# Kernel tuning notes

Hardware: AMD Instinct MI355X
Metric: run time of the kernel (lower is better)

## Reference

```python
import jax, jax.numpy as jnp
import numpy as np

N_STEPS = 8  # fixed-step Dormand-Prince RK45 steps replacing adaptive dopri5


def setup_inputs() -> dict:
    key = jax.random.key(0)
    ks = jax.random.split(key, 12)
    B, I, H = 16384, 128, 256
    s_ih = 1.0 / np.sqrt(I)
    s_hh = 1.0 / np.sqrt(H)
    return {
        "inputs": jax.random.normal(ks[0], (B, I), jnp.float32),
        "h0": jax.random.normal(ks[1], (B, H), jnp.float32),
        "c0": jax.random.normal(ks[2], (B, H), jnp.float32),
        "ts": jax.random.uniform(ks[3], (B,), jnp.float32),  # per-example end times in [0,1)
        "W_ih": jax.random.normal(ks[4], (4 * H, I), jnp.float32) * s_ih,
        "W_hh": jax.random.normal(ks[5], (4 * H, H), jnp.float32) * s_hh,
        "b_ih": jax.random.normal(ks[6], (4 * H,), jnp.float32) * s_hh,
        "b_hh": jax.random.normal(ks[7], (4 * H,), jnp.float32) * s_hh,
        "W1": jax.random.normal(ks[8], (H, H), jnp.float32) * s_hh,
        "b1": jax.random.normal(ks[9], (H,), jnp.float32) * s_hh,
        "W2": jax.random.normal(ks[10], (H, H), jnp.float32) * s_hh,
        "b2": jax.random.normal(ks[11], (H,), jnp.float32) * s_hh,
    }


def reference(inputs, h0, c0, ts, W_ih, W_hh, b_ih, b_hh, W1, b1, W2, b2):
    # ODE vector field: fc = Linear -> Tanh -> Linear (autonomous)
    def f(h):
        return jnp.tanh(h @ W1.T + b1) @ W2.T + b2

    dt = (ts / N_STEPS)[:, None]  # [B,1] per-example step size

    def rk45_step(h, _):
        k1 = f(h)
        k2 = f(h + dt * (0.2 * k1))
        k3 = f(h + dt * (3.0 / 40.0 * k1 + 9.0 / 40.0 * k2))
        k4 = f(h + dt * (44.0 / 45.0 * k1 - 56.0 / 15.0 * k2 + 32.0 / 9.0 * k3))
        k5 = f(h + dt * (19372.0 / 6561.0 * k1 - 25360.0 / 2187.0 * k2
                         + 64448.0 / 6561.0 * k3 - 212.0 / 729.0 * k4))
        k6 = f(h + dt * (9017.0 / 3168.0 * k1 - 355.0 / 33.0 * k2
                         + 46732.0 / 5247.0 * k3 + 49.0 / 176.0 * k4
                         - 5103.0 / 18656.0 * k5))
        h_new = h + dt * (35.0 / 384.0 * k1 + 500.0 / 1113.0 * k3
                          + 125.0 / 192.0 * k4 - 2187.0 / 6784.0 * k5
                          + 11.0 / 84.0 * k6)
        return h_new, None

    h_ode, _ = jax.lax.scan(rk45_step, h0, None, length=N_STEPS)

    def lstm_cell(x, h, c):
        gates = x @ W_ih.T + b_ih + h @ W_hh.T + b_hh  # [B,4H]
        i, fg, g, o = jnp.split(gates, 4, axis=-1)
        i = jax.nn.sigmoid(i)
        fg = jax.nn.sigmoid(fg)
        g = jnp.tanh(g)
        o = jax.nn.sigmoid(o)
        c_new = fg * c + i * g
        return o * jnp.tanh(c_new), c_new

    # two (weight-shared) LSTMCell applications as in the original forward
    h1, c1 = lstm_cell(inputs, h_ode, c0)
    h2, c2 = lstm_cell(inputs, h1, c1)
    return h2, c2
```

## Files before the change

kernel.cpp:

```cpp
#include <hip/hip_runtime.h>

#define B_TOT 16384
#define HD 256
#define ID 128
#define BT 32
#define NSTEP 8
#define YP 264
#define XP 136

typedef float    f32x4  __attribute__((ext_vector_type(4)));
typedef float    f32x16 __attribute__((ext_vector_type(16)));
typedef _Float16 f16x8  __attribute__((ext_vector_type(8)));
typedef _Float16 f16x4  __attribute__((ext_vector_type(4)));
typedef _Float16 f16x2  __attribute__((ext_vector_type(2)));

__device__ __forceinline__ float fast_rcp(float x){ return __builtin_amdgcn_rcpf(x); }
__device__ __forceinline__ float fast_exp2(float x){ return __builtin_amdgcn_exp2f(x); }
__device__ __forceinline__ float fast_tanh(float x){
  return 1.0f - 2.0f*fast_rcp(1.0f + fast_exp2(x*2.8853900817779268f));
}
__device__ __forceinline__ float fast_sigmoid(float x){
  return fast_rcp(1.0f + fast_exp2(x*-1.4426950408889634f));
}

__global__ void cvt_f32_f16(const float* __restrict__ src, _Float16* __restrict__ dst, int n4){
  int i = blockIdx.x*256 + threadIdx.x;
  if (i < n4){
    float4 v = ((const float4*)src)[i];
    f16x4 t = {(_Float16)v.x, (_Float16)v.y, (_Float16)v.z, (_Float16)v.w};
    *(f16x4*)(dst + (size_t)i*4) = t;
  }
}

#define KP(i) ((float)kpk[i][pk][hw])

__global__ __launch_bounds__(512, 2)
void ode_lstm(const float* __restrict__ inputs, const float* __restrict__ h0,
              const float* __restrict__ c0,     const float* __restrict__ ts,
              const float* __restrict__ b_ih,   const float* __restrict__ b_hh,
              const float* __restrict__ b1,     const float* __restrict__ b2,
              const _Float16* __restrict__ W1h, const _Float16* __restrict__ W2h,
              const _Float16* __restrict__ Wihh,const _Float16* __restrict__ Whhh,
              float* __restrict__ out)
{
  __shared__ __align__(16) _Float16 yl[BT*YP];
  __shared__ __align__(16) _Float16 ul[BT*YP];
  __shared__ __align__(16) _Float16 xl[BT*XP];
  __shared__ __align__(16) float b1l[HD], b2l[HD], bsl[4*HD];
  __shared__ float dtl[BT];

  const int tid  = threadIdx.x;
  const int wv   = tid >> 6;
  const int lane = tid & 63;
  const int l31  = lane & 31;
  const int hh   = lane >> 5;
  const int row0 = blockIdx.x * BT;
  const int cb   = wv*32 + hh*4;
  const int yrow = l31*YP + cb;

  #pragma unroll
  for (int it = 0; it < 2; ++it){
    int idx = tid + it*512;
    int r = idx >> 5, c4 = idx & 31;
    float4 v = ((const float4*)inputs)[(size_t)(row0 + r)*(ID/4) + c4];
    f16x4 t = {(_Float16)v.x, (_Float16)v.y, (_Float16)v.z, (_Float16)v.w};
    *(f16x4*)(xl + r*XP + c4*4) = t;
  }
  if (tid < HD){ b1l[tid] = b1[tid]; b2l[tid] = b2[tid]; }
  bsl[tid]       = b_ih[tid]       + b_hh[tid];
  bsl[tid + 512] = b_ih[tid + 512] + b_hh[tid + 512];
  if (tid < BT) dtl[tid] = ts[row0 + tid] * (1.0f/NSTEP);

  f16x8 W1f[16], W2f[16];
  {
    const _Float16* w1p = W1h + (size_t)(wv*32 + l31)*HD + hh*8;
    const _Float16* w2p = W2h + (size_t)(wv*32 + l31)*HD + hh*8;
    #pragma unroll
    for (int kt = 0; kt < 16; ++kt){
      W1f[kt] = *(const f16x8*)(w1p + kt*16);
      W2f[kt] = *(const f16x8*)(w2p + kt*16);
    }
  }

  f32x4 h4[4];
  #pragma unroll
  for (int g2 = 0; g2 < 4; ++g2){
    f32x4 hv = *(const f32x4*)(h0 + (size_t)(row0 + l31)*HD + cb + 8*g2);
    h4[g2] = hv;
    f16x4 t = {(_Float16)hv[0], (_Float16)hv[1], (_Float16)hv[2], (_Float16)hv[3]};
    *(f16x4*)(yl + yrow + 8*g2) = t;
  }
  __syncthreads();
  const float dtv = dtl[l31];

  auto gemm16 = [&](const f16x8 (&Wf)[16], const _Float16* __restrict__ act)->f32x16{
    f32x16 a = {};
    const _Float16* bp = act + l31*YP + hh*8;
    #pragma unroll
    for (int kt = 0; kt < 16; ++kt){
      f16x8 Bf = *(const f16x8*)(bp + kt*16);
      a = __builtin_amdgcn_mfma_f32_32x32x16_f16(Wf[kt], Bf, a, 0, 0, 0);
    }
    return a;
  };

  auto phase1 = [&](){
    f32x16 a = gemm16(W1f, yl);
    #pragma unroll
    for (int g2 = 0; g2 < 4; ++g2){
      f32x4 bv = *(const f32x4*)(b1l + cb + 8*g2);
      f16x4 uv;
      #pragma unroll
      for (int r3 = 0; r3 < 4; ++r3)
        uv[r3] = (_Float16)fast_tanh(a[g2*4 + r3] + bv[r3]);
      *(f16x4*)(ul + yrow + 8*g2) = uv;
    }
    __syncthreads();
  };

  #define STAGE(SIDX, YEXPR)                                              \
    phase1();                                                             \
    { f32x16 a2 = gemm16(W2f, ul);                                        \
      _Pragma("unroll")                                                   \
      for (int g2 = 0; g2 < 4; ++g2){                                     \
        f32x4 bv = *(const f32x4*)(b2l + cb + 8*g2);                      \
        f16x4 yv;                                                         \
        _Pragma("unroll")                                                 \
        for (int r3 = 0; r3 < 4; ++r3){                                   \
          const int r = g2*4 + r3; const int pk = r>>1; const int hw = r&1;\
          float kd = dtv*(a2[r] + bv[r3]);                                \
          if (SIDX < 5) kpk[SIDX][pk][hw] = (_Float16)kd;                 \
          yv[r3] = (_Float16)(YEXPR);                                     \
        }                                                                 \
        *(f16x4*)(yl + yrow + 8*g2) = yv;                                 \
      }                                                                   \
    }                                                                     \
    __syncthreads();

  #pragma unroll 1
  for (int step = 0; step < NSTEP; ++step){
    f16x2 kpk[5][8];

    STAGE(0, h4[g2][r3] + 0.2f*kd)
    STAGE(1, h4[g2][r3] + 0.075f*KP(0) + 0.225f*kd)
    STAGE(2, h4[g2][r3] + (44.0f/45.0f)*KP(0) + (-56.0f/15.0f)*KP(1)
                        + (32.0f/9.0f)*kd)
    STAGE(3, h4[g2][r3] + (19372.0f/6561.0f)*KP(0) + (-25360.0f/2187.0f)*KP(1)
                        + (64448.0f/6561.0f)*KP(2) + (-212.0f/729.0f)*kd)
    STAGE(4, h4[g2][r3] + (9017.0f/3168.0f)*KP(0) + (-355.0f/33.0f)*KP(1)
                        + (46732.0f/5247.0f)*KP(2) + (49.0f/176.0f)*KP(3)
                        + (-5103.0f/18656.0f)*kd)
    phase1();
    { f32x16 a2 = gemm16(W2f, ul);
      #pragma unroll
      for (int g2 = 0; g2 < 4; ++g2){
        f32x4 bv = *(const f32x4*)(b2l + cb + 8*g2);
        f16x4 yv;
        #pragma unroll
        for (int r3 = 0; r3 < 4; ++r3){
          const int r = g2*4 + r3; const int pk = r>>1; const int hw = r&1;
          float kd = dtv*(a2[r] + bv[r3]);
          float hn = h4[g2][r3] + (35.0f/384.0f)*KP(0) + (500.0f/1113.0f)*KP(2)
                   + (125.0f/192.0f)*KP(3) + (-2187.0f/6784.0f)*KP(4)
                   + (11.0f/84.0f)*kd;
          h4[g2][r3] = hn;
          yv[r3] = (_Float16)hn;
        }
        *(f16x4*)(yl + yrow + 8*g2) = yv;
      }
    }
    __syncthreads();
  }

  f32x16 agx[4] = {};
  {
    const _Float16* bp = xl + l31*XP + hh*8;
    #pragma unroll 2
    for (int kt = 0; kt < 8; ++kt){
      f16x8 Bf = *(const f16x8*)(bp + kt*16);
      #pragma unroll
      for (int g = 0; g < 4; ++g){
        f16x8 Af = *(const f16x8*)(Wihh + (size_t)(g*HD + wv*32 + l31)*ID + kt*16 + hh*8);
        agx[g] = __builtin_amdgcn_mfma_f32_32x32x16_f16(Af, Bf, agx[g], 0, 0, 0);
      }
    }
  }
  f32x4 c4[4];
  #pragma unroll
  for (int g2 = 0; g2 < 4; ++g2)
    c4[g2] = *(const f32x4*)(c0 + (size_t)(row0 + l31)*HD + cb + 8*g2);

  #pragma unroll 1
  for (int cell = 0; cell < 2; ++cell){
    f32x16 ag[4];
    #pragma unroll
    for (int g = 0; g < 4; ++g) ag[g] = agx[g];
    const _Float16* hsrc = (cell == 0) ? yl : ul;
    const _Float16* bp = hsrc + l31*YP + hh*8;
    #pragma unroll 2
    for (int kt = 0; kt < 16; ++kt){
      f16x8 Bf = *(const f16x8*)(bp + kt*16);
      #pragma unroll
      for (int g = 0; g < 4; ++g){
        f16x8 Af = *(const f16x8*)(Whhh + (size_t)(g*HD + wv*32 + l31)*HD + kt*16 + hh*8);
        ag[g] = __builtin_amdgcn_mfma_f32_32x32x16_f16(Af, Bf, ag[g], 0, 0, 0);
      }
    }
    #pragma unroll
    for (int g2 = 0; g2 < 4; ++g2){
      f32x4 bi = *(const f32x4*)(bsl + 0*HD + cb + 8*g2);
      f32x4 bf = *(const f32x4*)(bsl + 1*HD + cb + 8*g2);
      f32x4 bg = *(const f32x4*)(bsl + 2*HD + cb + 8*g2);
      f32x4 bo = *(const f32x4*)(bsl + 3*HD + cb + 8*g2);
      f16x4 hv; f32x4 ho, co;
      #pragma unroll
      for (int r3 = 0; r3 < 4; ++r3){
        const int r = g2*4 + r3;
        float iv = fast_sigmoid(ag[0][r] + bi[r3]);
        float fv = fast_sigmoid(ag[1][r] + bf[r3]);
        float gv = fast_tanh   (ag[2][r] + bg[r3]);
        float ov = fast_sigmoid(ag[3][r] + bo[r3]);
        float cn = fv*c4[g2][r3] + iv*gv;
        c4[g2][r3] = cn;
        float hn = ov*fast_tanh(cn);
        hv[r3] = (_Float16)hn; ho[r3] = hn; co[r3] = cn;
      }
      if (cell == 0){
        *(f16x4*)(ul + yrow + 8*g2) = hv;
      } else {
        size_t o = (size_t)(row0 + l31)*HD + cb + 8*g2;
        *(f32x4*)(out + o) = ho;
        *(f32x4*)(out + (size_t)B_TOT*HD + o) = co;
      }
    }
    if (cell == 0) __syncthreads();
  }
}

extern "C" void kernel_launch(void* const* d_in, const int* in_sizes, int n_in,
                              void* d_out, int out_size, void* d_ws, size_t ws_size,
                              hipStream_t stream) {
  (void)in_sizes; (void)n_in; (void)out_size; (void)ws_size;
  const float* inputs = (const float*)d_in[0];
  const float* h0     = (const float*)d_in[1];
  const float* c0     = (const float*)d_in[2];
  const float* ts     = (const float*)d_in[3];
  const float* W_ih   = (const float*)d_in[4];
  const float* W_hh   = (const float*)d_in[5];
  const float* b_ih   = (const float*)d_in[6];
  const float* b_hh   = (const float*)d_in[7];
  const float* W1     = (const float*)d_in[8];
  const float* b1     = (const float*)d_in[9];
  const float* W2     = (const float*)d_in[10];
  const float* b2     = (const float*)d_in[11];
  float* out = (float*)d_out;

  _Float16* wsh  = (_Float16*)d_ws;
  _Float16* W1h  = wsh;
  _Float16* W2h  = wsh + 65536;
  _Float16* Wihh = wsh + 131072;
  _Float16* Whhh = wsh + 262144;

  cvt_f32_f16<<<64,  256, 0, stream>>>(W1,   W1h,  16384);
  cvt_f32_f16<<<64,  256, 0, stream>>>(W2,   W2h,  16384);
  cvt_f32_f16<<<128, 256, 0, stream>>>(W_ih, Wihh, 32768);
  cvt_f32_f16<<<256, 256, 0, stream>>>(W_hh, Whhh, 65536);

  ode_lstm<<<B_TOT/BT, 512, 0, stream>>>(inputs, h0, c0, ts, b_ih, b_hh, b1, b2,
                                         W1h, W2h, Wihh, Whhh, out);
}
```

Measured before the change: 413.1 us.

## Interleave two 32-row sub-batches to overlap GEMM with epilogue per block

Each block now handles 64 rows as two 32-row halves, A and B. It software-pipelines the RK stages so the MFMA GEMM for one half is issued alongside the elementwise epilogue (tanh, RK combination) of the other half. The fp32 ODE state moves from registers into LDS, freeing VGPRs for a second set of stage accumulators. The input/LSTM LDS buffers are aliased onto the h-state buffers after the ODE loop. This aims to hide epilogue latency and halve the number of blocks, at the cost of more LDS use and extra LDS traffic for the state.

Measured after the change: 660.1 us. +59.8%, slower.

```diff
diff --git a/kernel.cpp b/kernel.cpp
--- a/kernel.cpp
+++ b/kernel.cpp
@@ -3,10 +3,11 @@
 #define B_TOT 16384
 #define HD 256
 #define ID 128
-#define BT 32
+#define BT 64
 #define NSTEP 8
 #define YP 264
 #define XP 136
+#define HP 260
 
 typedef float    f32x4  __attribute__((ext_vector_type(4)));
 typedef float    f32x16 __attribute__((ext_vector_type(16)));
@@ -32,7 +33,63 @@
   }
 }
 
-#define KP(i) ((float)kpk[i][pk][hw])
+#define KPF(K,i) ((float)K[i][pk][hw])
+
+#define YX0(K) (hv[r3] + 0.2f*kd)
+#define YX1(K) (hv[r3] + 0.075f*KPF(K,0) + 0.225f*kd)
+#define YX2(K) (hv[r3] + (44.0f/45.0f)*KPF(K,0) + (-56.0f/15.0f)*KPF(K,1) + (32.0f/9.0f)*kd)
+#define YX3(K) (hv[r3] + (19372.0f/6561.0f)*KPF(K,0) + (-25360.0f/2187.0f)*KPF(K,1) \
+                        + (64448.0f/6561.0f)*KPF(K,2) + (-212.0f/729.0f)*kd)
+#define YX4(K) (hv[r3] + (9017.0f/3168.0f)*KPF(K,0) + (-355.0f/33.0f)*KPF(K,1) \
+                        + (46732.0f/5247.0f)*KPF(K,2) + (49.0f/176.0f)*KPF(K,3) \
+                        + (-5103.0f/18656.0f)*kd)
+#define YX5(K) (hv[r3] + (35.0f/384.0f)*KPF(K,0) + (500.0f/1113.0f)*KPF(K,2) \
+                        + (125.0f/192.0f)*KPF(K,3) + (-2187.0f/6784.0f)*KPF(K,4) \
+                        + (11.0f/84.0f)*kd)
+
+#define EPI2(ACC, YB, HS, K, DTV, SIDX, YXM)                               \
+  { _Pragma("unroll")                                                      \
+    for (int g2 = 0; g2 < 4; ++g2){                                        \
+      f32x4 hv = *(const f32x4*)(HS + hoff + 8*g2);                        \
+      f32x4 bv = *(const f32x4*)(b2l + cb + 8*g2);                         \
+      f16x4 yv; f32x4 hnv;                                                 \
+      _Pragma("unroll")                                                    \
+      for (int r3 = 0; r3 < 4; ++r3){                                      \
+        const int r = g2*4 + r3; const int pk = r>>1; const int hw = r&1;  \
+        float kd = DTV*(ACC[r] + bv[r3]);                                  \
+        if ((SIDX) < 5) K[(SIDX)<5?(SIDX):0][pk][hw] = (_Float16)kd;       \
+        float yn = YXM(K);                                                 \
+        hnv[r3] = yn;                                                      \
+        yv[r3] = (_Float16)yn;                                             \
+      }                                                                    \
+      if ((SIDX) == 5) *(f32x4*)(HS + hoff + 8*g2) = hnv;                  \
+      *(f16x4*)(YB + yoff + 8*g2) = yv;                                    \
+    }                                                                      \
+  }
+
+#define EPI1(ACC, YB)                                                      \
+  { _Pragma("unroll")                                                      \
+    for (int g2 = 0; g2 < 4; ++g2){                                        \
+      f32x4 bv = *(const f32x4*)(b1l + cb + 8*g2);                         \
+      f16x4 uv;                                                            \
+      _Pragma("unroll")                                                    \
+      for (int r3 = 0; r3 < 4; ++r3)                                       \
+        uv[r3] = (_Float16)fast_tanh(ACC[g2*4+r3] + bv[r3]);               \
+      *(f16x4*)(YB + yoff + 8*g2) = uv;                                    \
+    }                                                                      \
+  }
+
+#define SEGBCD(S)                                                          \
+  aB = gemm16(W1f, ybB);  EPI1(aA, ybA);  __syncthreads();                 \
+  aA = gemm16(W2f, ybA);  EPI1(aB, ybB);  __syncthreads();                 \
+  aB = gemm16(W2f, ybB);  EPI2(aA, ybA, hslA, kpkA, dtvA, S, YX##S);       \
+  __syncthreads();
+
+#define STAGE4(S, SP)                                                      \
+  aA = gemm16(W1f, ybA);                                                   \
+  EPI2(aB, ybB, hslB, kpkB, dtvB, SP, YX##SP);                             \
+  __syncthreads();                                                         \
+  SEGBCD(S)
 
 __global__ __launch_bounds__(512, 2)
 void ode_lstm(const float* __restrict__ inputs, const float* __restrict__ h0,
@@ -43,10 +100,9 @@
               const _Float16* __restrict__ Wihh,const _Float16* __restrict__ Whhh,
               float* __restrict__ out)
 {
-  __shared__ __align__(16) _Float16 yl[BT*YP];
-  __shared__ __align__(16) _Float16 ul[BT*YP];
-  __shared__ __align__(16) _Float16 xl[BT*XP];
-  __shared__ __align__(16) float b1l[HD], b2l[HD], bsl[4*HD];
+  __shared__ __align__(16) _Float16 ybA[32*YP], ybB[32*YP];
+  __shared__ __align__(16) float    hslA[32*HP], hslB[32*HP];
+  __shared__ __align__(16) float    b1l[HD], b2l[HD], bsl[4*HD];
   __shared__ float dtl[BT];
 
   const int tid  = threadIdx.x;
@@ -56,16 +112,9 @@
   const int hh   = lane >> 5;
   const int row0 = blockIdx.x * BT;
   const int cb   = wv*32 + hh*4;
-  const int yrow = l31*YP + cb;
-
-  #pragma unroll
-  for (int it = 0; it < 2; ++it){
-    int idx = tid + it*512;
-    int r = idx >> 5, c4 = idx & 31;
-    float4 v = ((const float4*)inputs)[(size_t)(row0 + r)*(ID/4) + c4];
-    f16x4 t = {(_Float16)v.x, (_Float16)v.y, (_Float16)v.z, (_Float16)v.w};
-    *(f16x4*)(xl + r*XP + c4*4) = t;
-  }
+  const int yoff = l31*YP + cb;
+  const int hoff = l31*HP + cb;
+
   if (tid < HD){ b1l[tid] = b1[tid]; b2l[tid] = b2[tid]; }
   bsl[tid]       = b_ih[tid]       + b_hh[tid];
   bsl[tid + 512] = b_ih[tid + 512] + b_hh[tid + 512];
@@ -82,16 +131,19 @@
     }
   }
 
-  f32x4 h4[4];
   #pragma unroll
   for (int g2 = 0; g2 < 4; ++g2){
-    f32x4 hv = *(const f32x4*)(h0 + (size_t)(row0 + l31)*HD + cb + 8*g2);
-    h4[g2] = hv;
-    f16x4 t = {(_Float16)hv[0], (_Float16)hv[1], (_Float16)hv[2], (_Float16)hv[3]};
-    *(f16x4*)(yl + yrow + 8*g2) = t;
-  }
-  __syncthreads();
-  const float dtv = dtl[l31];
+    f32x4 ha = *(const f32x4*)(h0 + (size_t)(row0 + l31)*HD + cb + 8*g2);
+    f32x4 hb = *(const f32x4*)(h0 + (size_t)(row0 + 32 + l31)*HD + cb + 8*g2);
+    *(f32x4*)(hslA + hoff + 8*g2) = ha;
+    *(f32x4*)(hslB + hoff + 8*g2) = hb;
+    f16x4 ta = {(_Float16)ha[0],(_Float16)ha[1],(_Float16)ha[2],(_Float16)ha[3]};
+    f16x4 tb = {(_Float16)hb[0],(_Float16)hb[1],(_Float16)hb[2],(_Float16)hb[3]};
+    *(f16x4*)(ybA + yoff + 8*g2) = ta;
+    *(f16x4*)(ybB + yoff + 8*g2) = tb;
+  }
+  __syncthreads();
+  const float dtvA = dtl[l31], dtvB = dtl[32 + l31];
 
   auto gemm16 = [&](const f16x8 (&Wf)[16], const _Float16* __restrict__ act)->f32x16{
     f32x16 a = {};
@@ -104,136 +156,110 @@
     return a;
   };
 
-  auto phase1 = [&](){
-    f32x16 a = gemm16(W1f, yl);
-    #pragma unroll
-    for (int g2 = 0; g2 < 4; ++g2){
-      f32x4 bv = *(const f32x4*)(b1l + cb + 8*g2);
-      f16x4 uv;
-      #pragma unroll
-      for (int r3 = 0; r3 < 4; ++r3)
-        uv[r3] = (_Float16)fast_tanh(a[g2*4 + r3] + bv[r3]);
-      *(f16x4*)(ul + yrow + 8*g2) = uv;
-    }
-    __syncthreads();
-  };
-
-  #define STAGE(SIDX, YEXPR)                                              \
-    phase1();                                                             \
-    { f32x16 a2 = gemm16(W2f, ul);                                        \
-      _Pragma("unroll")                                                   \
-      for (int g2 = 0; g2 < 4; ++g2){                                     \
-        f32x4 bv = *(const f32x4*)(b2l + cb + 8*g2);                      \
-        f16x4 yv;                                                         \
-        _Pragma("unroll")                                                 \
-        for (int r3 = 0; r3 < 4; ++r3){                                   \
-          const int r = g2*4 + r3; const int pk = r>>1; const int hw = r&1;\
-          float kd = dtv*(a2[r] + bv[r3]);                                \
-          if (SIDX < 5) kpk[SIDX][pk][hw] = (_Float16)kd;                 \
-          yv[r3] = (_Float16)(YEXPR);                                     \
-        }                                                                 \
-        *(f16x4*)(yl + yrow + 8*g2) = yv;                                 \
-      }                                                                   \
-    }                                                                     \
-    __syncthreads();
+  f32x16 aA, aB;
+  f16x2 kpkA[5][8], kpkB[5][8];
 
   #pragma unroll 1
   for (int step = 0; step < NSTEP; ++step){
-    f16x2 kpk[5][8];
-
-    STAGE(0, h4[g2][r3] + 0.2f*kd)
-    STAGE(1, h4[g2][r3] + 0.075f*KP(0) + 0.225f*kd)
-    STAGE(2, h4[g2][r3] + (44.0f/45.0f)*KP(0) + (-56.0f/15.0f)*KP(1)
-                        + (32.0f/9.0f)*kd)
-    STAGE(3, h4[g2][r3] + (19372.0f/6561.0f)*KP(0) + (-25360.0f/2187.0f)*KP(1)
-                        + (64448.0f/6561.0f)*KP(2) + (-212.0f/729.0f)*kd)
-    STAGE(4, h4[g2][r3] + (9017.0f/3168.0f)*KP(0) + (-355.0f/33.0f)*KP(1)
-                        + (46732.0f/5247.0f)*KP(2) + (49.0f/176.0f)*KP(3)
-                        + (-5103.0f/18656.0f)*kd)
-    phase1();
-    { f32x16 a2 = gemm16(W2f, ul);
+    aA = gemm16(W1f, ybA);
+    if (step > 0) { EPI2(aB, ybB, hslB, kpkB, dtvB, 5, YX5); }
+    __syncthreads();
+    SEGBCD(0)
+    STAGE4(1, 0)
+    STAGE4(2, 1)
+    STAGE4(3, 2)
+    STAGE4(4, 3)
+    STAGE4(5, 4)
+  }
+  { EPI2(aB, ybB, hslB, kpkB, dtvB, 5, YX5); }
+  __syncthreads();
+
+  _Float16* xA  = (_Float16*)hslA;
+  _Float16* xB  = (_Float16*)hslB;
+  _Float16* h1A = ((_Float16*)hslA) + 32*XP;
+  _Float16* h1B = ((_Float16*)hslB) + 32*XP;
+
+  #pragma unroll
+  for (int it = 0; it < 4; ++it){
+    int idx = tid + it*512;
+    int r = idx >> 5, c4 = idx & 31;
+    float4 v = ((const float4*)inputs)[(size_t)(row0 + r)*(ID/4) + c4];
+    f16x4 t = {(_Float16)v.x, (_Float16)v.y, (_Float16)v.z, (_Float16)v.w};
+    _Float16* xd = (r < 32) ? xA : xB;
+    *(f16x4*)(xd + (r & 31)*XP + c4*4) = t;
+  }
+  __syncthreads();
+
+  #pragma unroll 1
+  for (int sb = 0; sb < 2; ++sb){
+    const _Float16* xs  = sb ? xB  : xA;
+    const _Float16* hod = sb ? ybB : ybA;
+    _Float16*       h1  = sb ? h1B : h1A;
+    const int rbase = row0 + sb*32;
+
+    f32x16 agx[4] = {};
+    {
+      const _Float16* bp = xs + l31*XP + hh*8;
+      #pragma unroll 2
+      for (int kt = 0; kt < 8; ++kt){
+        f16x8 Bf = *(const f16x8*)(bp + kt*16);
+        #pragma unroll
+        for (int g = 0; g < 4; ++g){
+          f16x8 Af = *(const f16x8*)(Wihh + (size_t)(g*HD + wv*32 + l31)*ID + kt*16 + hh*8);
+          agx[g] = __builtin_amdgcn_mfma_f32_32x32x16_f16(Af, Bf, agx[g], 0, 0, 0);
+        }
+      }
+    }
+    f32x4 c4v[4];
+    #pragma unroll
+    for (int g2 = 0; g2 < 4; ++g2)
+      c4v[g2] = *(const f32x4*)(c0 + (size_t)(rbase + l31)*HD + cb + 8*g2);
+
+    #pragma unroll 1
+    for (int cell = 0; cell < 2; ++cell){
+      f32x16 ag[4];
+      #pragma unroll
+      for (int g = 0; g < 4; ++g) ag[g] = agx[g];
+      const _Float16* hb = (cell == 0) ? hod : h1;
+      const _Float16* bp = hb + l31*YP + hh*8;
+      #pragma unroll 2
+      for (int kt = 0; kt < 16; ++kt){
+        f16x8 Bf = *(const f16x8*)(bp + kt*16);
+        #pragma unroll
+        for (int g = 0; g < 4; ++g){
+          f16x8 Af = *(const f16x8*)(Whhh + (size_t)(g*HD + wv*32 + l31)*HD + kt*16 + hh*8);
+          ag[g] = __builtin_amdgcn_mfma_f32_32x32x16_f16(Af, Bf, ag[g], 0, 0, 0);
+        }
+      }
       #pragma unroll
       for (int g2 = 0; g2 < 4; ++g2){
-        f32x4 bv = *(const f32x4*)(b2l + cb + 8*g2);
-        f16x4 yv;
+        f32x4 bi = *(const f32x4*)(bsl + 0*HD + cb + 8*g2);
+        f32x4 bf = *(const f32x4*)(bsl + 1*HD + cb + 8*g2);
+        f32x4 bg = *(const f32x4*)(bsl + 2*HD + cb + 8*g2);
+        f32x4 bo = *(const f32x4*)(bsl + 3*HD + cb + 8*g2);
+        f16x4 hv16; f32x4 ho, co;
         #pragma unroll
         for (int r3 = 0; r3 < 4; ++r3){
-          const int r = g2*4 + r3; const int pk = r>>1; const int hw = r&1;
-          float kd = dtv*(a2[r] + bv[r3]);
-          float hn = h4[g2][r3] + (35.0f/384.0f)*KP(0) + (500.0f/1113.0f)*KP(2)
-                   + (125.0f/192.0f)*KP(3) + (-2187.0f/6784.0f)*KP(4)
-                   + (11.0f/84.0f)*kd;
-          h4[g2][r3] = hn;
-          yv[r3] = (_Float16)hn;
-        }
-        *(f16x4*)(yl + yrow + 8*g2) = yv;
+          const int r = g2*4 + r3;
+          float iv = fast_sigmoid(ag[0][r] + bi[r3]);
+          float fv = fast_sigmoid(ag[1][r] + bf[r3]);
+          float gv = fast_tanh   (ag[2][r] + bg[r3]);
+          float ov = fast_sigmoid(ag[3][r] + bo[r3]);
+          float cn = fv*c4v[g2][r3] + iv*gv;
+          c4v[g2][r3] = cn;
+          float hn = ov*fast_tanh(cn);
+          hv16[r3] = (_Float16)hn; ho[r3] = hn; co[r3] = cn;
+        }
+        if (cell == 0){
+          *(f16x4*)(h1 + yoff + 8*g2) = hv16;
+        } else {
+          size_t o = (size_t)(rbase + l31)*HD + cb + 8*g2;
+          *(f32x4*)(out + o) = ho;
+          *(f32x4*)(out + (size_t)B_TOT*HD + o) = co;
+        }
       }
-    }
-    __syncthreads();
-  }
-
-  f32x16 agx[4] = {};
-  {
-    const _Float16* bp = xl + l31*XP + hh*8;
-    #pragma unroll 2
-    for (int kt = 0; kt < 8; ++kt){
-      f16x8 Bf = *(const f16x8*)(bp + kt*16);
-      #pragma unroll
-      for (int g = 0; g < 4; ++g){
-        f16x8 Af = *(const f16x8*)(Wihh + (size_t)(g*HD + wv*32 + l31)*ID + kt*16 + hh*8);
-        agx[g] = __builtin_amdgcn_mfma_f32_32x32x16_f16(Af, Bf, agx[g], 0, 0, 0);
-      }
-    }
-  }
-  f32x4 c4[4];
-  #pragma unroll
-  for (int g2 = 0; g2 < 4; ++g2)
-    c4[g2] = *(const f32x4*)(c0 + (size_t)(row0 + l31)*HD + cb + 8*g2);
-
-  #pragma unroll 1
-  for (int cell = 0; cell < 2; ++cell){
-    f32x16 ag[4];
-    #pragma unroll
-    for (int g = 0; g < 4; ++g) ag[g] = agx[g];
-    const _Float16* hsrc = (cell == 0) ? yl : ul;
-    const _Float16* bp = hsrc + l31*YP + hh*8;
-    #pragma unroll 2
-    for (int kt = 0; kt < 16; ++kt){
-      f16x8 Bf = *(const f16x8*)(bp + kt*16);
-      #pragma unroll
-      for (int g = 0; g < 4; ++g){
-        f16x8 Af = *(const f16x8*)(Whhh + (size_t)(g*HD + wv*32 + l31)*HD + kt*16 + hh*8);
-        ag[g] = __builtin_amdgcn_mfma_f32_32x32x16_f16(Af, Bf, ag[g], 0, 0, 0);
-      }
-    }
-    #pragma unroll
-    for (int g2 = 0; g2 < 4; ++g2){
-      f32x4 bi = *(const f32x4*)(bsl + 0*HD + cb + 8*g2);
-      f32x4 bf = *(const f32x4*)(bsl + 1*HD + cb + 8*g2);
-      f32x4 bg = *(const f32x4*)(bsl + 2*HD + cb + 8*g2);
-      f32x4 bo = *(const f32x4*)(bsl + 3*HD + cb + 8*g2);
-      f16x4 hv; f32x4 ho, co;
-      #pragma unroll
-      for (int r3 = 0; r3 < 4; ++r3){
-        const int r = g2*4 + r3;
-        float iv = fast_sigmoid(ag[0][r] + bi[r3]);
-        float fv = fast_sigmoid(ag[1][r] + bf[r3]);
-        float gv = fast_tanh   (ag[2][r] + bg[r3]);
-        float ov = fast_sigmoid(ag[3][r] + bo[r3]);
-        float cn = fv*c4[g2][r3] + iv*gv;
-        c4[g2][r3] = cn;
-        float hn = ov*fast_tanh(cn);
-        hv[r3] = (_Float16)hn; ho[r3] = hn; co[r3] = cn;
-      }
-      if (cell == 0){
-        *(f16x4*)(ul + yrow + 8*g2) = hv;
-      } else {
-        size_t o = (size_t)(row0 + l31)*HD + cb + 8*g2;
-        *(f32x4*)(out + o) = ho;
-        *(f32x4*)(out + (size_t)B_TOT*HD + o) = co;
-      }
-    }
-    if (cell == 0) __syncthreads();
+      if (cell == 0) __syncthreads();
+    }
   }
 }
 
```
